# Kernel optimization log

Measured on AMD Instinct MI355X. Metric: run time of the kernel, lower is better.

## Reference

```python
import jax, jax.numpy as jnp
import numpy as np

B, L, V, E, U = 128, 64, 50000, 256, 256  # units = lstm_dim/2 = 256


def setup_inputs() -> dict:
    key = jax.random.key(0)
    ks = jax.random.split(key, 12)
    iq = jax.random.randint(ks[0], (B, L), 0, V, dtype=jnp.int32)
    ir = jax.random.randint(ks[1], (B, L), 0, V, dtype=jnp.int32)
    ql = jax.random.randint(ks[2], (B,), 1, L + 1, dtype=jnp.int32)
    rl = jax.random.randint(ks[3], (B,), 1, L + 1, dtype=jnp.int32)
    # all off-diagonal (i, j) pairs in row-major order (negative mask = 1 - eye)
    qi, ri = np.nonzero(1 - np.eye(B, dtype=np.int32))
    return {
        "input_queries": iq, "input_replies": ir,
        "query_lengths": ql, "reply_lengths": rl,
        "neg_q_idx": jnp.asarray(qi, jnp.int32), "neg_r_idx": jnp.asarray(ri, jnp.int32),
        "embeddings": jax.random.normal(ks[4], (V, E), jnp.float32) * 0.02,
        "gate_k": jax.random.normal(ks[5], (4, 2, E + U, 2 * U), jnp.float32) * 0.05,
        "gate_b": jnp.ones((4, 2, 2 * U), jnp.float32),
        "cand_k": jax.random.normal(ks[6], (4, 2, E + U, U), jnp.float32) * 0.05,
        "cand_b": jnp.zeros((4, 2, U), jnp.float32),
        "w1": jax.random.normal(ks[7], (4 * 4 * U + 1, 1024), jnp.float32) * 0.02,
        "b1": jnp.zeros((1024,), jnp.float32),
        "w2": jax.random.normal(ks[8], (1024, 2), jnp.float32) * 0.05,
        "b2": jnp.zeros((2,), jnp.float32),
    }


def _gru(x, h, k, b, kc, bc):
    # TF GRUCell: r,u = sigmoid([x,h]@k + b); c = tanh([x, r*h]@kc + bc); h' = u*h + (1-u)*c
    rz = jax.nn.sigmoid(jnp.concatenate([x, h], 1) @ k + b)
    r, z = jnp.split(rz, 2, axis=1)
    c = jnp.tanh(jnp.concatenate([x, r * h], 1) @ kc + bc)
    return z * h + (1.0 - z) * c


def _encode(emb, lengths, gk, gb, ck, cb):
    # 2-layer stacked GRU over time with sequence-length masking; returns concat of
    # both layers' final states ([B, 2U]) as in MultiRNNCell + dynamic_rnn.
    b, l, _ = emb.shape
    mask = jnp.arange(l)[None, :] < lengths[:, None]  # [B, L]

    def step(carry, inp):
        h1, h2 = carry
        x, m = inp
        h1n = _gru(x, h1, gk[0], gb[0], ck[0], cb[0])
        h2n = _gru(h1n, h2, gk[1], gb[1], ck[1], cb[1])
        m = m[:, None]
        return (jnp.where(m, h1n, h1), jnp.where(m, h2n, h2)), None

    init = (jnp.zeros((b, U), emb.dtype), jnp.zeros((b, U), emb.dtype))
    (h1, h2), _ = jax.lax.scan(step, init, (emb.transpose(1, 0, 2), mask.T))
    return jnp.concatenate([h1, h2], axis=1)


def _rev_seq(emb, lengths):
    # per-row reversal of the first `length` timesteps (tf.reverse_sequence)
    t = jnp.arange(emb.shape[1])[None, :]
    idx = jnp.where(t < lengths[:, None], lengths[:, None] - 1 - t, t)
    return jnp.take_along_axis(emb, idx[:, :, None], axis=1)


def reference(input_queries, input_replies, query_lengths, reply_lengths,
              neg_q_idx, neg_r_idx, embeddings, gate_k, gate_b, cand_k, cand_b,
              w1, b1, w2, b2):
    qe = embeddings[input_queries]  # [B, L, E]
    re_ = embeddings[input_replies]
    q_fw = _encode(qe, query_lengths, gate_k[0], gate_b[0], cand_k[0], cand_b[0])
    q_bw = _encode(_rev_seq(qe, query_lengths), query_lengths,
                   gate_k[1], gate_b[1], cand_k[1], cand_b[1])
    r_fw = _encode(re_, reply_lengths, gate_k[2], gate_b[2], cand_k[2], cand_b[2])
    r_bw = _encode(_rev_seq(re_, reply_lengths), reply_lengths,
                   gate_k[3], gate_b[3], cand_k[3], cand_b[3])
    Q = jnp.concatenate([q_fw, q_bw], 1)  # [B, 4U]
    R = jnp.concatenate([r_fw, r_bw], 1)

    dist = Q @ R.T                                    # [B, B]
    pos_d = jnp.diagonal(dist)[:, None]               # [B, 1]
    neg_d = dist[neg_q_idx, neg_r_idx][:, None]        # [N, 1]
    pos_in = jnp.concatenate([Q, pos_d, Q - R, Q * R, R], 1)
    Qn, Rn = Q[neg_q_idx], R[neg_r_idx]
    neg_in = jnp.concatenate([Qn, neg_d, Qn - Rn, Qn * Rn, Rn], 1)

    x = jnp.concatenate([pos_in, neg_in], 0)           # [B + N, 4*4U + 1]
    h = jax.nn.relu(x @ w1 + b1)
    return h @ w2 + b2                                 # logits [B + N, 2]
```

## Files before the change

### kernel.cpp

```cpp
#include <hip/hip_runtime.h>
#include <hip/hip_fp16.h>
#include <cmath>

typedef _Float16 h2 __attribute__((ext_vector_type(2)));
typedef _Float16 f16x8 __attribute__((ext_vector_type(8)));
typedef float f32x4 __attribute__((ext_vector_type(4)));

#define MFMA16 __builtin_amdgcn_mfma_f32_16x16x32_f16

#if defined(__has_builtin)
#if __has_builtin(__builtin_amdgcn_fdot2)
#define HAS_FDOT2 1
#endif
#endif

__device__ __forceinline__ float fdot2f(h2 a, h2 b, float c) {
#ifdef HAS_FDOT2
    return __builtin_amdgcn_fdot2(a, b, c, false);
#else
    c = fmaf((float)a[0], (float)b[0], c);
    return fmaf((float)a[1], (float)b[1], c);
#endif
}

__device__ __forceinline__ float sigm(float x) { return 1.0f / (1.0f + expf(-x)); }
__device__ __forceinline__ unsigned short f16b(float x) {
    _Float16 h = (_Float16)x; return __builtin_bit_cast(unsigned short, h);
}

__global__ __launch_bounds__(256) void conv_all(
    const float* __restrict__ gate_k, const float* __restrict__ cand_k,
    const float* __restrict__ w1,
    float* __restrict__ gkh, float* __restrict__ ckh,
    f16x8* __restrict__ wB, float* __restrict__ wcomb)
{
    int i = blockIdx.x * 256 + threadIdx.x;
    if (i < 8 * 256 * 512) {
        int col = i & 511, kp = (i >> 9) & 255, e2 = i >> 17;
        const float* src = gate_k + ((size_t)e2 * 512 + 2 * kp) * 512 + col;
        h2 v; v[0] = (_Float16)src[0]; v[1] = (_Float16)src[512];
        gkh[i] = __builtin_bit_cast(float, v);
    }
    if (i < 8 * 256 * 256) {
        int col = i & 255, kp = (i >> 8) & 255, e2 = i >> 16;
        const float* src = cand_k + ((size_t)e2 * 512 + 2 * kp) * 256 + col;
        h2 v; v[0] = (_Float16)src[0]; v[1] = (_Float16)src[256];
        ckh[i] = __builtin_bit_cast(float, v);
    }
    if (i < 32 * 64 * 64) {
        int l = i & 63, nt = (i >> 6) & 63, kt = i >> 12;
        int k0 = kt*32 + ((l >> 4) << 3);
        int n  = (nt << 4) + (l & 15);
        const float* src = w1 + (size_t)(2049 + k0) * 1024 + n;
        f16x8 v;
        #pragma unroll
        for (int j = 0; j < 8; ++j) v[j] = (_Float16)src[(size_t)j * 1024];
        wB[i] = v;
    }
    {
        int mat = i >> 20;
        int e = i & 1048575;
        const float* wmain = mat ? (w1 + (size_t)3073 * 1024) : w1;
        const float* wdiff = w1 + (size_t)1025 * 1024;
        float sgn = mat ? -1.f : 1.f;
        wcomb[i] = wmain[e] + sgn * wdiff[e];
    }
}

__device__ __forceinline__ void gate_partial_h(
    const _Float16* in0f, float* pbuf, const float* __restrict__ gk, int tid)
{
    int cg = tid & 127, q = tid >> 7;
    int c0 = cg * 4;
    const float* gp = gk + (size_t)(q * 32) * 512 + c0;
    const _Float16* xp = in0f + q * 32 * 4;
    float4 A0 = {0.f,0.f,0.f,0.f}, A1 = {0.f,0.f,0.f,0.f};
    #pragma unroll 8
    for (int i = 0; i < 32; ++i) {
        float4 wf = *(const float4*)(gp + (size_t)i * 512);
        float2 xf = *(const float2*)(xp + i * 4);
        h2 w0 = __builtin_bit_cast(h2, wf.x), w1 = __builtin_bit_cast(h2, wf.y);
        h2 w2 = __builtin_bit_cast(h2, wf.z), w3 = __builtin_bit_cast(h2, wf.w);
        h2 x0 = __builtin_bit_cast(h2, xf.x), x1 = __builtin_bit_cast(h2, xf.y);
        A0.x = fdot2f(x0, w0, A0.x); A0.y = fdot2f(x0, w1, A0.y);
        A0.z = fdot2f(x0, w2, A0.z); A0.w = fdot2f(x0, w3, A0.w);
        A1.x = fdot2f(x1, w0, A1.x); A1.y = fdot2f(x1, w1, A1.y);
        A1.z = fdot2f(x1, w2, A1.z); A1.w = fdot2f(x1, w3, A1.w);
    }
    *(float4*)&pbuf[(q * 2 + 0) * 512 + c0] = A0;
    *(float4*)&pbuf[(q * 2 + 1) * 512 + c0] = A1;
}

__device__ __forceinline__ void cand_partial_h(
    const _Float16* in0f, float* pbuf, const float* __restrict__ ck, int tid)
{
    int cg = tid & 63, q = tid >> 6;
    int c0 = cg * 4;
    const float* cp = ck + (size_t)(q * 16) * 256 + c0;
    const _Float16* xp = in0f + q * 16 * 4;
    float4 A0 = {0.f,0.f,0.f,0.f}, A1 = {0.f,0.f,0.f,0.f};
    #pragma unroll 8
    for (int i = 0; i < 16; ++i) {
        float4 wf = *(const float4*)(cp + (size_t)i * 256);
        float2 xf = *(const float2*)(xp + i * 4);
        h2 w0 = __builtin_bit_cast(h2, wf.x), w1 = __builtin_bit_cast(h2, wf.y);
        h2 w2 = __builtin_bit_cast(h2, wf.z), w3 = __builtin_bit_cast(h2, wf.w);
        h2 x0 = __builtin_bit_cast(h2, xf.x), x1 = __builtin_bit_cast(h2, xf.y);
        A0.x = fdot2f(x0, w0, A0.x); A0.y = fdot2f(x0, w1, A0.y);
        A0.z = fdot2f(x0, w2, A0.z); A0.w = fdot2f(x0, w3, A0.w);
        A1.x = fdot2f(x1, w0, A1.x); A1.y = fdot2f(x1, w1, A1.y);
        A1.z = fdot2f(x1, w2, A1.z); A1.w = fdot2f(x1, w3, A1.w);
    }
    *(float4*)&pbuf[(q * 2 + 0) * 256 + c0] = A0;
    *(float4*)&pbuf[(q * 2 + 1) * 256 + c0] = A1;
}

__global__ __launch_bounds__(1024, 4) void gru_encode(
    const int* __restrict__ iq, const int* __restrict__ ir,
    const int* __restrict__ ql, const int* __restrict__ rl,
    const float* __restrict__ emb,
    const float* __restrict__ gkh, const float* __restrict__ gate_b,
    const float* __restrict__ ckh, const float* __restrict__ cand_b,
    float* __restrict__ Qo, float* __restrict__ Ro)
{
    int bid = blockIdx.x;
    int xcd = bid & 7;
    int enc = xcd >> 1;
    int chunk = (xcd & 1) * 32 + (bid >> 3);
    int b0 = chunk * 2;
    int tid = threadIdx.x;

    const int* toks = (enc < 2) ? iq : ir;
    const int* lens = (enc < 2) ? ql : rl;
    const bool bw = (enc & 1);

    const float* gk1 = gkh + (size_t)(enc * 2 + 0) * 131072;
    const float* gk2 = gkh + (size_t)(enc * 2 + 1) * 131072;
    const float* gb1 = gate_b + (enc * 2 + 0) * 512;
    const float* gb2 = gate_b + (enc * 2 + 1) * 512;
    const float* ck1 = ckh + (size_t)(enc * 2 + 0) * 65536;
    const float* ck2 = ckh + (size_t)(enc * 2 + 1) * 65536;
    const float* cb1 = cand_b + (enc * 2 + 0) * 256;
    const float* cb2 = cand_b + (enc * 2 + 1) * 256;

    __shared__ __align__(16) _Float16 in0fA[256 * 4];
    __shared__ __align__(16) _Float16 in0fB[256 * 4];
    __shared__ float pbuf[8192];
    __shared__ float h1rt[2][256];
    __shared__ float h2rt[2][256];
    __shared__ float gzt[2][256];
    __shared__ int len_s[2];

    if (tid < 512) { int r = tid >> 8, c = tid & 255; h1rt[r][c] = 0.f; h2rt[r][c] = 0.f; }
    if (tid < 2) len_s[tid] = lens[b0 + tid];
    __syncthreads();
    int maxlen = max(len_s[0], len_s[1]);
    if (tid < 256) {
        int kp = tid >> 1, rr = tid & 1;
        int len = len_s[rr];
        int tok = toks[(b0 + rr) * 64 + (bw ? (len - 1) : 0)];
        float2 xv = *(const float2*)(emb + (size_t)tok * 256 + 2 * kp);
        h2 v; v[0] = (_Float16)xv.x; v[1] = (_Float16)xv.y;
        *(float*)(in0fA + kp * 4 + rr * 2) = __builtin_bit_cast(float, v);
    } else if (tid < 512) {
        int m = (tid - 256) >> 1, rr = tid & 1;
        *(unsigned int*)(in0fA + (128 + m) * 4 + rr * 2) = 0u;
    }
    __syncthreads();

    for (int t = 0; t < maxlen; ++t) {
        gate_partial_h(in0fA, pbuf, gk1, tid);
        __syncthreads();
        if (tid < 512) {
            int c = tid & 255, r = tid >> 8;
            float s0 = gb1[c], s1 = gb1[256 + c];
            #pragma unroll
            for (int q = 0; q < 8; ++q) {
                s0 += pbuf[(q * 2 + r) * 512 + c];
                s1 += pbuf[(q * 2 + r) * 512 + c + 256];
            }
            float rh = sigm(s0) * h1rt[r][c];
            gzt[r][c] = sigm(s1);
            in0fA[((256 + c) >> 1) * 4 + r * 2 + (c & 1)] = (_Float16)rh;
        }
        __syncthreads();
        cand_partial_h(in0fA, pbuf, ck1, tid);
        __syncthreads();
        if (tid < 512) {
            int c = tid & 255, r = tid >> 8;
            float s = cb1[c];
            #pragma unroll
            for (int q = 0; q < 16; ++q) s += pbuf[(q * 2 + r) * 256 + c];
            float cv = tanhf(s);
            float z = gzt[r][c];
            float hn = fmaf(z, h1rt[r][c] - cv, cv);
            float hm = (t < len_s[r]) ? hn : h1rt[r][c];
            h1rt[r][c] = hm;
            in0fB[(c >> 1) * 4 + r * 2 + (c & 1)]         = (_Float16)hn;
            in0fB[((256 + c) >> 1) * 4 + r * 2 + (c & 1)] = (_Float16)h2rt[r][c];
            in0fA[((256 + c) >> 1) * 4 + r * 2 + (c & 1)] = (_Float16)hm;
        }
        __syncthreads();

        gate_partial_h(in0fB, pbuf, gk2, tid);
        __syncthreads();
        if (tid < 512) {
            int c = tid & 255, r = tid >> 8;
            float s0 = gb2[c], s1 = gb2[256 + c];
            #pragma unroll
            for (int q = 0; q < 8; ++q) {
                s0 += pbuf[(q * 2 + r) * 512 + c];
                s1 += pbuf[(q * 2 + r) * 512 + c + 256];
            }
            float rh = sigm(s0) * h2rt[r][c];
            gzt[r][c] = sigm(s1);
            in0fB[((256 + c) >> 1) * 4 + r * 2 + (c & 1)] = (_Float16)rh;
        }
        __syncthreads();
        cand_partial_h(in0fB, pbuf, ck2, tid);
        __syncthreads();
        if (tid < 512) {
            int c = tid & 255, r = tid >> 8;
            float s = cb2[c];
            #pragma unroll
            for (int q = 0; q < 16; ++q) s += pbuf[(q * 2 + r) * 256 + c];
            float cv = tanhf(s);
            float z = gzt[r][c];
            float hn = fmaf(z, h2rt[r][c] - cv, cv);
            if (t < len_s[r]) h2rt[r][c] = hn;
        }
        if (tid < 256) {
            int t2 = t + 1;
            if (t2 < 64) {
                int kp = tid >> 1, rr = tid & 1;
                int len = len_s[rr];
                int tt = bw ? ((t2 < len) ? (len - 1 - t2) : t2) : t2;
                int tok = toks[(b0 + rr) * 64 + tt];
                float2 xv = *(const float2*)(emb + (size_t)tok * 256 + 2 * kp);
                h2 v; v[0] = (_Float16)xv.x; v[1] = (_Float16)xv.y;
                *(float*)(in0fA + kp * 4 + rr * 2) = __builtin_bit_cast(float, v);
            }
        }
        __syncthreads();
    }

    if (tid < 512) {
        int r = tid >> 8, c = tid & 255;
        float* outp = (enc < 2) ? Qo : Ro;
        int off = (enc & 1) ? 512 : 0;
        outp[(size_t)(b0 + r) * 1024 + off + c]       = h1rt[r][c];
        outp[(size_t)(b0 + r) * 1024 + off + 256 + c] = h2rt[r][c];
    }
}

__global__ __launch_bounds__(256) void ab_kernel(
    const float* __restrict__ Q, const float* __restrict__ R,
    const float* __restrict__ wcomb, float* __restrict__ A, float* __restrict__ Bv)
{
    int nb = blockIdx.x, rb = blockIdx.y, mat = blockIdx.z;
    int tid = threadIdx.x;
    int n = nb * 256 + tid;
    int r0 = rb * 4;
    const float* src = mat ? R : Q;
    const float* wc  = wcomb + (size_t)mat * 1048576;

    __shared__ float Qs[4][64];
    float acc[4] = {0.f, 0.f, 0.f, 0.f};

    for (int k0 = 0; k0 < 1024; k0 += 64) {
        __syncthreads();
        {
            int rr = tid >> 6, kk = tid & 63;
            Qs[rr][kk] = src[(size_t)(r0 + rr) * 1024 + k0 + kk];
        }
        __syncthreads();
        for (int kk = 0; kk < 64; ++kk) {
            float w = wc[(size_t)(k0 + kk) * 1024 + n];
            #pragma unroll
            for (int r = 0; r < 4; ++r)
                acc[r] = fmaf(Qs[r][kk], w, acc[r]);
        }
    }
    float* dst = mat ? Bv : A;
    #pragma unroll
    for (int r = 0; r < 4; ++r)
        dst[(size_t)(r0 + r) * 1024 + n] = acc[r];
}

__global__ __launch_bounds__(512, 2) void pair_gemm(
    const float* __restrict__ Q, const float* __restrict__ R,
    const float* __restrict__ Aq, const float* __restrict__ Bv,
    const int* __restrict__ nqi, const int* __restrict__ nri,
    const f16x8* __restrict__ wB,
    const float* __restrict__ w1, const float* __restrict__ b1,
    const float* __restrict__ w2, float* __restrict__ partial)
{
    int bm = blockIdx.x, bn = blockIdx.y;
    int tid = threadIdx.x, w = tid >> 6, l = tid & 63;
    __shared__ __align__(16) unsigned short As[4096];
    __shared__ float red[2048];
    __shared__ float dred[4][128];
    __shared__ int qis[128], ris[128];
    __shared__ float dsv[128];
    if (tid < 128) {
        int p = bm*128 + tid;
        int qi = (p < 128) ? p : nqi[p-128];
        int ri = (p < 128) ? p : nri[p-128];
        qis[tid] = qi; ris[tid] = ri;
    }
    __syncthreads();

    int srow = tid & 127, skg = tid >> 7;
    const float* qrow = Q + (size_t)qis[srow]*1024 + skg*8;
    const float* rrow = R + (size_t)ris[srow]*1024 + skg*8;

    float4 qa = *(const float4*)(qrow);
    float4 qb = *(const float4*)(qrow + 4);
    float4 ra = *(const float4*)(rrow);
    float4 rb = *(const float4*)(rrow + 4);

    f32x4 acc[8];
    #pragma unroll
    for (int m = 0; m < 8; ++m) acc[m] = (f32x4){0.f,0.f,0.f,0.f};
    float dacc = 0.f;

    for (int kt = 0; kt < 32; ++kt) {
        float p0 = qa.x*ra.x, p1 = qa.y*ra.y, p2 = qa.z*ra.z, p3 = qa.w*ra.w;
        float p4 = qb.x*rb.x, p5 = qb.y*rb.y, p6 = qb.z*rb.z, p7 = qb.w*rb.w;
        dacc += ((p0 + p1) + (p2 + p3)) + ((p4 + p5) + (p6 + p7));
        f16x8 prod;
        prod[0]=(_Float16)p0; prod[1]=(_Float16)p1;
        prod[2]=(_Float16)p2; prod[3]=(_Float16)p3;
        prod[4]=(_Float16)p4; prod[5]=(_Float16)p5;
        prod[6]=(_Float16)p6; prod[7]=(_Float16)p7;
        __syncthreads();
        ((f16x8*)As)[srow*4 + (skg ^ (srow & 3))] = prod;
        __syncthreads();
        if (kt + 1 < 32) {
            qa = *(const float4*)(qrow + (kt+1)*32);
            qb = *(const float4*)(qrow + (kt+1)*32 + 4);
            ra = *(const float4*)(rrow + (kt+1)*32);
            rb = *(const float4*)(rrow + (kt+1)*32 + 4);
        }
        f16x8 bf = wB[((size_t)kt*64 + bn*8 + w)*64 + l];
        #pragma unroll
        for (int mt = 0; mt < 8; ++mt) {
            f16x8 af = ((const f16x8*)As)[(mt*16 + (l & 15))*4 + ((l >> 4) ^ (l & 3))];
            acc[mt] = MFMA16(af, bf, acc[mt], 0, 0, 0);
        }
    }

    dred[skg][srow] = dacc;
    __syncthreads();
    if (tid < 128)
        dsv[tid] = (dred[0][tid] + dred[1][tid]) + (dred[2][tid] + dred[3][tid]);
    __syncthreads();

    int col = bn*128 + w*16 + (l & 15);
    float wd  = w1[(size_t)1024*1024 + col];
    float b1v = b1[col];
    float w20 = w2[col*2], w21 = w2[col*2 + 1];
    #pragma unroll
    for (int mt = 0; mt < 8; ++mt) {
        float po0[4], po1[4];
        #pragma unroll
        for (int j = 0; j < 4; ++j) {
            int lr = mt*16 + (l >> 4)*4 + j;
            float h = acc[mt][j]
                    + Aq[(size_t)qis[lr]*1024 + col]
                    + Bv[(size_t)ris[lr]*1024 + col]
                    + dsv[lr]*wd + b1v;
            h = fmaxf(h, 0.f);
            po0[j] = h * w20; po1[j] = h * w21;
        }
        #pragma unroll
        for (int s = 1; s < 16; s <<= 1) {
            #pragma unroll
            for (int j = 0; j < 4; ++j) {
                po0[j] += __shfl_xor(po0[j], s, 64);
                po1[j] += __shfl_xor(po1[j], s, 64);
            }
        }
        if ((l & 15) == 0) {
            #pragma unroll
            for (int j = 0; j < 4; ++j) {
                int row = mt*16 + (l >> 4)*4 + j;
                red[(w*128 + row)*2 + 0] = po0[j];
                red[(w*128 + row)*2 + 1] = po1[j];
            }
        }
    }
    __syncthreads();
    if (tid < 256) {
        int row = tid >> 1, cc = tid & 1;
        float s = 0.f;
        #pragma unroll
        for (int ww = 0; ww < 8; ++ww) s += red[(ww*128 + row)*2 + cc];
        partial[((size_t)bn*16384 + bm*128 + row)*2 + cc] = s;
    }
}

__global__ void final_reduce(const float* __restrict__ partial,
                             const float* __restrict__ b2, float* __restrict__ out)
{
    int gidx = blockIdx.x * 256 + threadIdx.x;
    int p = gidx >> 1, c = gidx & 1;
    float s = b2[c];
    #pragma unroll
    for (int nt = 0; nt < 8; ++nt)
        s += partial[((size_t)nt * 16384 + p) * 2 + c];
    out[gidx] = s;
}

extern "C" void kernel_launch(void* const* d_in, const int* in_sizes, int n_in,
                              void* d_out, int out_size, void* d_ws, size_t ws_size,
                              hipStream_t stream) {
    const int*   iq     = (const int*)d_in[0];
    const int*   ir     = (const int*)d_in[1];
    const int*   ql     = (const int*)d_in[2];
    const int*   rl     = (const int*)d_in[3];
    const int*   nqi    = (const int*)d_in[4];
    const int*   nri    = (const int*)d_in[5];
    const float* emb    = (const float*)d_in[6];
    const float* gate_k = (const float*)d_in[7];
    const float* gate_b = (const float*)d_in[8];
    const float* cand_k = (const float*)d_in[9];
    const float* cand_b = (const float*)d_in[10];
    const float* w1     = (const float*)d_in[11];
    const float* b1     = (const float*)d_in[12];
    const float* w2     = (const float*)d_in[13];
    const float* b2     = (const float*)d_in[14];
    float* out = (float*)d_out;
    float* ws  = (float*)d_ws;

    float* Q       = ws;
    float* R       = ws + 131072;
    float* A       = ws + 262144;
    float* Bv      = ws + 393216;
    float* partial = ws + 540672;
    float* gkh     = ws + 1064960;
    float* ckh     = ws + 2113536;
    f16x8* wB      = (f16x8*)(ws + 2637824);
    float* wcomb   = ws + 3162112;

    conv_all<<<8192, 256, 0, stream>>>(gate_k, cand_k, w1, gkh, ckh, wB, wcomb);
    gru_encode<<<256, 1024, 0, stream>>>(iq, ir, ql, rl, emb, gkh, gate_b,
                                         ckh, cand_b, Q, R);
    ab_kernel<<<dim3(4, 32, 2), 256, 0, stream>>>(Q, R, wcomb, A, Bv);
    pair_gemm<<<dim3(128, 8), 512, 0, stream>>>(Q, R, A, Bv, nqi, nri,
                                                wB, w1, b1, w2, partial);
    final_reduce<<<128, 256, 0, stream>>>(partial, b2, out);
}
```

Measured before the change: 1.084 ms.

## Hoist layer-1 input projections out of GRU recurrence into a batched MFMA GEMM

Adds a precompute_x kernel that gathers embeddings and computes the input-side gate and candidate projections for all timesteps with MFMA, storing them as fp16. The recurrent kernel then only multiplies by the hidden-state half of the layer-1 weights, which halves the serial per-step matvec work for that layer. The wcomb precompute is also removed and its combination is folded into ab_kernel's weight loads. The new path depends on workspace size, adds an extra launch and an fp16 intermediate buffer, and doubles weight reads in ab_kernel.

```diff
diff --git a/kernel.cpp b/kernel.cpp
--- a/kernel.cpp
+++ b/kernel.cpp
@@ -31,8 +31,7 @@
 __global__ __launch_bounds__(256) void conv_all(
     const float* __restrict__ gate_k, const float* __restrict__ cand_k,
     const float* __restrict__ w1,
-    float* __restrict__ gkh, float* __restrict__ ckh,
-    f16x8* __restrict__ wB, float* __restrict__ wcomb)
+    float* __restrict__ gkh, float* __restrict__ ckh, f16x8* __restrict__ wB)
 {
     int i = blockIdx.x * 256 + threadIdx.x;
     if (i < 8 * 256 * 512) {
@@ -57,13 +56,77 @@
         for (int j = 0; j < 8; ++j) v[j] = (_Float16)src[(size_t)j * 1024];
         wB[i] = v;
     }
-    {
-        int mat = i >> 20;
-        int e = i & 1048575;
-        const float* wmain = mat ? (w1 + (size_t)3073 * 1024) : w1;
-        const float* wdiff = w1 + (size_t)1025 * 1024;
-        float sgn = mat ? -1.f : 1.f;
-        wcomb[i] = wmain[e] + sgn * wdiff[e];
+}
+
+__global__ __launch_bounds__(512) void precompute_x(
+    const int* __restrict__ iq, const int* __restrict__ ir,
+    const int* __restrict__ ql, const int* __restrict__ rl,
+    const float* __restrict__ emb,
+    const float* __restrict__ gate_k, const float* __restrict__ cand_k,
+    _Float16* __restrict__ xg, _Float16* __restrict__ xc)
+{
+    int mtile = blockIdx.x;
+    int nt    = blockIdx.y;
+    int enc   = blockIdx.z;
+    int tid = threadIdx.x, w = tid >> 6, l = tid & 63;
+    const int* toks = (enc < 2) ? iq : ir;
+    const int* lens = (enc < 2) ? ql : rl;
+    const bool bw = (enc & 1);
+    const bool isg = (nt < 4);
+    int n0 = isg ? nt * 128 : (nt - 4) * 128;
+    int nstride = isg ? 512 : 256;
+    const float* W = isg ? (gate_k + (size_t)(enc * 2) * 512 * 512)
+                         : (cand_k + (size_t)(enc * 2) * 512 * 256);
+    _Float16* dst = isg ? (xg + (size_t)enc * 8192 * 512)
+                        : (xc + (size_t)enc * 8192 * 256);
+
+    __shared__ int tok_l[128];
+    __shared__ __align__(16) unsigned short As[4096];
+
+    if (tid < 128) {
+        int b = mtile * 2 + (tid >> 6), t = tid & 63;
+        int len = lens[b];
+        int tt = bw ? ((t < len) ? (len - 1 - t) : t) : t;
+        tok_l[tid] = toks[b * 64 + tt];
+    }
+    __syncthreads();
+
+    int srow = tid & 127, skg = tid >> 7;
+
+    f32x4 acc[8];
+    #pragma unroll
+    for (int m = 0; m < 8; ++m) acc[m] = (f32x4){0.f, 0.f, 0.f, 0.f};
+
+    for (int kt = 0; kt < 8; ++kt) {
+        const float* es = emb + (size_t)tok_l[srow] * 256 + kt * 32 + skg * 8;
+        float4 e0 = *(const float4*)es;
+        float4 e1 = *(const float4*)(es + 4);
+        f16x8 av;
+        av[0]=(_Float16)e0.x; av[1]=(_Float16)e0.y; av[2]=(_Float16)e0.z; av[3]=(_Float16)e0.w;
+        av[4]=(_Float16)e1.x; av[5]=(_Float16)e1.y; av[6]=(_Float16)e1.z; av[7]=(_Float16)e1.w;
+        __syncthreads();
+        ((f16x8*)As)[srow * 4 + (skg ^ (srow & 3))] = av;
+        __syncthreads();
+
+        const float* wp = W + (size_t)(kt * 32 + (l >> 4) * 8) * nstride + n0 + w * 16 + (l & 15);
+        f16x8 bf;
+        #pragma unroll
+        for (int j = 0; j < 8; ++j) bf[j] = (_Float16)wp[(size_t)j * nstride];
+        #pragma unroll
+        for (int mt = 0; mt < 8; ++mt) {
+            f16x8 af = ((const f16x8*)As)[(mt * 16 + (l & 15)) * 4 + ((l >> 4) ^ (l & 3))];
+            acc[mt] = MFMA16(af, bf, acc[mt], 0, 0, 0);
+        }
+    }
+
+    int ncol = n0 + w * 16 + (l & 15);
+    #pragma unroll
+    for (int mt = 0; mt < 8; ++mt) {
+        #pragma unroll
+        for (int j = 0; j < 4; ++j) {
+            int m = mtile * 128 + mt * 16 + (l >> 4) * 4 + j;
+            dst[(size_t)m * nstride + ncol] = (_Float16)acc[mt][j];
+        }
     }
 }
 
@@ -91,6 +154,30 @@
     *(float4*)&pbuf[(q * 2 + 1) * 512 + c0] = A1;
 }
 
+__device__ __forceinline__ void gate_partial_h_half(
+    const _Float16* in0f, float* pbuf, const float* __restrict__ gk, int tid)
+{
+    int cg = tid & 127, q = tid >> 7;
+    int c0 = cg * 4;
+    const float* gp = gk + (size_t)(128 + q * 16) * 512 + c0;
+    const _Float16* xp = in0f + (128 + q * 16) * 4;
+    float4 A0 = {0.f,0.f,0.f,0.f}, A1 = {0.f,0.f,0.f,0.f};
+    #pragma unroll
+    for (int i = 0; i < 16; ++i) {
+        float4 wf = *(const float4*)(gp + (size_t)i * 512);
+        float2 xf = *(const float2*)(xp + i * 4);
+        h2 w0 = __builtin_bit_cast(h2, wf.x), w1 = __builtin_bit_cast(h2, wf.y);
+        h2 w2 = __builtin_bit_cast(h2, wf.z), w3 = __builtin_bit_cast(h2, wf.w);
+        h2 x0 = __builtin_bit_cast(h2, xf.x), x1 = __builtin_bit_cast(h2, xf.y);
+        A0.x = fdot2f(x0, w0, A0.x); A0.y = fdot2f(x0, w1, A0.y);
+        A0.z = fdot2f(x0, w2, A0.z); A0.w = fdot2f(x0, w3, A0.w);
+        A1.x = fdot2f(x1, w0, A1.x); A1.y = fdot2f(x1, w1, A1.y);
+        A1.z = fdot2f(x1, w2, A1.z); A1.w = fdot2f(x1, w3, A1.w);
+    }
+    *(float4*)&pbuf[(q * 2 + 0) * 512 + c0] = A0;
+    *(float4*)&pbuf[(q * 2 + 1) * 512 + c0] = A1;
+}
+
 __device__ __forceinline__ void cand_partial_h(
     const _Float16* in0f, float* pbuf, const float* __restrict__ ck, int tid)
 {
@@ -115,6 +202,150 @@
     *(float4*)&pbuf[(q * 2 + 1) * 256 + c0] = A1;
 }
 
+__device__ __forceinline__ void cand_partial_h_half(
+    const _Float16* in0f, float* pbuf, const float* __restrict__ ck, int tid)
+{
+    int cg = tid & 63, q = tid >> 6;
+    int c0 = cg * 4;
+    const float* cp = ck + (size_t)(128 + q * 8) * 256 + c0;
+    const _Float16* xp = in0f + (128 + q * 8) * 4;
+    float4 A0 = {0.f,0.f,0.f,0.f}, A1 = {0.f,0.f,0.f,0.f};
+    #pragma unroll
+    for (int i = 0; i < 8; ++i) {
+        float4 wf = *(const float4*)(cp + (size_t)i * 256);
+        float2 xf = *(const float2*)(xp + i * 4);
+        h2 w0 = __builtin_bit_cast(h2, wf.x), w1 = __builtin_bit_cast(h2, wf.y);
+        h2 w2 = __builtin_bit_cast(h2, wf.z), w3 = __builtin_bit_cast(h2, wf.w);
+        h2 x0 = __builtin_bit_cast(h2, xf.x), x1 = __builtin_bit_cast(h2, xf.y);
+        A0.x = fdot2f(x0, w0, A0.x); A0.y = fdot2f(x0, w1, A0.y);
+        A0.z = fdot2f(x0, w2, A0.z); A0.w = fdot2f(x0, w3, A0.w);
+        A1.x = fdot2f(x1, w0, A1.x); A1.y = fdot2f(x1, w1, A1.y);
+        A1.z = fdot2f(x1, w2, A1.z); A1.w = fdot2f(x1, w3, A1.w);
+    }
+    *(float4*)&pbuf[(q * 2 + 0) * 256 + c0] = A0;
+    *(float4*)&pbuf[(q * 2 + 1) * 256 + c0] = A1;
+}
+
+__global__ __launch_bounds__(1024, 4) void gru_encode_px(
+    const int* __restrict__ ql, const int* __restrict__ rl,
+    const float* __restrict__ gkh, const float* __restrict__ gate_b,
+    const float* __restrict__ ckh, const float* __restrict__ cand_b,
+    const _Float16* __restrict__ xg, const _Float16* __restrict__ xc,
+    float* __restrict__ Qo, float* __restrict__ Ro)
+{
+    int bid = blockIdx.x;
+    int xcd = bid & 7;
+    int enc = xcd >> 1;
+    int chunk = (xcd & 1) * 32 + (bid >> 3);
+    int b0 = chunk * 2;
+    int tid = threadIdx.x;
+
+    const int* lens = (enc < 2) ? ql : rl;
+
+    const float* gk1 = gkh + (size_t)(enc * 2 + 0) * 131072;
+    const float* gk2 = gkh + (size_t)(enc * 2 + 1) * 131072;
+    const float* gb1 = gate_b + (enc * 2 + 0) * 512;
+    const float* gb2 = gate_b + (enc * 2 + 1) * 512;
+    const float* ck1 = ckh + (size_t)(enc * 2 + 0) * 65536;
+    const float* ck2 = ckh + (size_t)(enc * 2 + 1) * 65536;
+    const float* cb1 = cand_b + (enc * 2 + 0) * 256;
+    const float* cb2 = cand_b + (enc * 2 + 1) * 256;
+    const _Float16* xgE = xg + (size_t)enc * 8192 * 512;
+    const _Float16* xcE = xc + (size_t)enc * 8192 * 256;
+
+    __shared__ __align__(16) _Float16 in0fA[256 * 4];
+    __shared__ __align__(16) _Float16 in0fB[256 * 4];
+    __shared__ float pbuf[8192];
+    __shared__ float h1rt[2][256];
+    __shared__ float h2rt[2][256];
+    __shared__ float gzt[2][256];
+    __shared__ int len_s[2];
+
+    if (tid < 512) { int r = tid >> 8, c = tid & 255; h1rt[r][c] = 0.f; h2rt[r][c] = 0.f; }
+    if (tid < 2) len_s[tid] = lens[b0 + tid];
+    if (tid < 256) {
+        int m = tid >> 1, rr = tid & 1;
+        *(unsigned int*)(in0fA + (128 + m) * 4 + rr * 2) = 0u;
+    }
+    __syncthreads();
+    int maxlen = max(len_s[0], len_s[1]);
+
+    for (int t = 0; t < maxlen; ++t) {
+        gate_partial_h_half(in0fA, pbuf, gk1, tid);
+        __syncthreads();
+        if (tid < 512) {
+            int c = tid & 255, r = tid >> 8;
+            const _Float16* xgp = xgE + ((size_t)(b0 + r) * 64 + t) * 512;
+            float s0 = gb1[c] + (float)xgp[c];
+            float s1 = gb1[256 + c] + (float)xgp[256 + c];
+            #pragma unroll
+            for (int q = 0; q < 8; ++q) {
+                s0 += pbuf[(q * 2 + r) * 512 + c];
+                s1 += pbuf[(q * 2 + r) * 512 + c + 256];
+            }
+            float rh = sigm(s0) * h1rt[r][c];
+            gzt[r][c] = sigm(s1);
+            in0fA[((256 + c) >> 1) * 4 + r * 2 + (c & 1)] = (_Float16)rh;
+        }
+        __syncthreads();
+        cand_partial_h_half(in0fA, pbuf, ck1, tid);
+        __syncthreads();
+        if (tid < 512) {
+            int c = tid & 255, r = tid >> 8;
+            const _Float16* xcp = xcE + ((size_t)(b0 + r) * 64 + t) * 256;
+            float s = cb1[c] + (float)xcp[c];
+            #pragma unroll
+            for (int q = 0; q < 16; ++q) s += pbuf[(q * 2 + r) * 256 + c];
+            float cv = tanhf(s);
+            float z = gzt[r][c];
+            float hn = fmaf(z, h1rt[r][c] - cv, cv);
+            float hm = (t < len_s[r]) ? hn : h1rt[r][c];
+            h1rt[r][c] = hm;
+            in0fB[(c >> 1) * 4 + r * 2 + (c & 1)]         = (_Float16)hn;
+            in0fB[((256 + c) >> 1) * 4 + r * 2 + (c & 1)] = (_Float16)h2rt[r][c];
+            in0fA[((256 + c) >> 1) * 4 + r * 2 + (c & 1)] = (_Float16)hm;
+        }
+        __syncthreads();
+
+        gate_partial_h(in0fB, pbuf, gk2, tid);
+        __syncthreads();
+        if (tid < 512) {
+            int c = tid & 255, r = tid >> 8;
+            float s0 = gb2[c], s1 = gb2[256 + c];
+            #pragma unroll
+            for (int q = 0; q < 8; ++q) {
+                s0 += pbuf[(q * 2 + r) * 512 + c];
+                s1 += pbuf[(q * 2 + r) * 512 + c + 256];
+            }
+            float rh = sigm(s0) * h2rt[r][c];
+            gzt[r][c] = sigm(s1);
+            in0fB[((256 + c) >> 1) * 4 + r * 2 + (c & 1)] = (_Float16)rh;
+        }
+        __syncthreads();
+        cand_partial_h(in0fB, pbuf, ck2, tid);
+        __syncthreads();
+        if (tid < 512) {
+            int c = tid & 255, r = tid >> 8;
+            float s = cb2[c];
+            #pragma unroll
+            for (int q = 0; q < 16; ++q) s += pbuf[(q * 2 + r) * 256 + c];
+            float cv = tanhf(s);
+            float z = gzt[r][c];
+            float hn = fmaf(z, h2rt[r][c] - cv, cv);
+            if (t < len_s[r]) h2rt[r][c] = hn;
+        }
+        __syncthreads();
+    }
+
+    if (tid < 512) {
+        int r = tid >> 8, c = tid & 255;
+        float* outp = (enc < 2) ? Qo : Ro;
+        int off = (enc & 1) ? 512 : 0;
+        outp[(size_t)(b0 + r) * 1024 + off + c]       = h1rt[r][c];
+        outp[(size_t)(b0 + r) * 1024 + off + 256 + c] = h2rt[r][c];
+    }
+}
+
 __global__ __launch_bounds__(1024, 4) void gru_encode(
     const int* __restrict__ iq, const int* __restrict__ ir,
     const int* __restrict__ ql, const int* __restrict__ rl,
@@ -255,14 +486,16 @@
 
 __global__ __launch_bounds__(256) void ab_kernel(
     const float* __restrict__ Q, const float* __restrict__ R,
-    const float* __restrict__ wcomb, float* __restrict__ A, float* __restrict__ Bv)
+    const float* __restrict__ w1, float* __restrict__ A, float* __restrict__ Bv)
 {
     int nb = blockIdx.x, rb = blockIdx.y, mat = blockIdx.z;
     int tid = threadIdx.x;
     int n = nb * 256 + tid;
     int r0 = rb * 4;
-    const float* src = mat ? R : Q;
-    const float* wc  = wcomb + (size_t)mat * 1048576;
+    const float* src   = mat ? R : Q;
+    const float* wmain = mat ? (w1 + (size_t)3073 * 1024) : w1;
+    const float* wdiff = w1 + (size_t)1025 * 1024;
+    float sgn = mat ? -1.f : 1.f;
 
     __shared__ float Qs[4][64];
     float acc[4] = {0.f, 0.f, 0.f, 0.f};
@@ -275,7 +508,8 @@
         }
         __syncthreads();
         for (int kk = 0; kk < 64; ++kk) {
-            float w = wc[(size_t)(k0 + kk) * 1024 + n];
+            size_t row = (size_t)(k0 + kk) * 1024 + n;
+            float w = wmain[row] + sgn * wdiff[row];
             #pragma unroll
             for (int r = 0; r < 4; ++r)
                 acc[r] = fmaf(Qs[r][kk], w, acc[r]);
@@ -441,12 +675,21 @@
     float* gkh     = ws + 1064960;
     float* ckh     = ws + 2113536;
     f16x8* wB      = (f16x8*)(ws + 2637824);
-    float* wcomb   = ws + 3162112;
-
-    conv_all<<<8192, 256, 0, stream>>>(gate_k, cand_k, w1, gkh, ckh, wB, wcomb);
-    gru_encode<<<256, 1024, 0, stream>>>(iq, ir, ql, rl, emb, gkh, gate_b,
-                                         ckh, cand_b, Q, R);
-    ab_kernel<<<dim3(4, 32, 2), 256, 0, stream>>>(Q, R, wcomb, A, Bv);
+    _Float16* xg   = (_Float16*)(ws + 3162112);
+    _Float16* xc   = (_Float16*)(ws + 11550720);
+    const size_t WS_NEEDED = (size_t)15745024 * 4;
+
+    conv_all<<<4096, 256, 0, stream>>>(gate_k, cand_k, w1, gkh, ckh, wB);
+    if (ws_size >= WS_NEEDED) {
+        precompute_x<<<dim3(64, 6, 4), 512, 0, stream>>>(iq, ir, ql, rl, emb,
+                                                         gate_k, cand_k, xg, xc);
+        gru_encode_px<<<256, 1024, 0, stream>>>(ql, rl, gkh, gate_b, ckh, cand_b,
+                                                xg, xc, Q, R);
+    } else {
+        gru_encode<<<256, 1024, 0, stream>>>(iq, ir, ql, rl, emb, gkh, gate_b,
+                                             ckh, cand_b, Q, R);
+    }
+    ab_kernel<<<dim3(4, 32, 2), 256, 0, stream>>>(Q, R, w1, A, Bv);
     pair_gemm<<<dim3(128, 8), 512, 0, stream>>>(Q, R, A, Bv, nqi, nri,
                                                 wB, w1, b1, w2, partial);
     final_reduce<<<128, 256, 0, stream>>>(partial, b2, out);
```

After: 1.486 ms. 1.37x slower.
